# Optimization experiments

Hardware: AMD Instinct MI355X
Metric: run time of the kernel (lower is better)

Reference implementation:

```python
import jax, jax.numpy as jnp
import numpy as np

FEAT = 128 * 4 * 4   # 2048, from input_size=(64,128,4,4)
NCLS = 20            # hard-coded n_classes
S = 0.31             # threshold margin from forward()


def setup_inputs() -> dict:
    key = jax.random.key(0)
    kx, ke, kc, kf = jax.random.split(key, 4)
    x = jax.random.normal(kx, (16384, 128, 4, 4), dtype=jnp.float32)
    # encoder stub: linear 2048 -> 2048
    W_enc = jax.random.normal(ke, (FEAT, FEAT), dtype=jnp.float32) * 0.02
    b_enc = jnp.zeros((FEAT,), dtype=jnp.float32)
    # classifier: linear 2048 -> 20
    W_cls = jax.random.normal(kc, (FEAT, NCLS), dtype=jnp.float32) * 0.02
    b_cls = jnp.zeros((NCLS,), dtype=jnp.float32)
    # flow classification head: linear 2048 -> 20 (produces flow_logits)
    W_fl = jax.random.normal(kf, (FEAT, NCLS), dtype=jnp.float32) * 0.02
    b_fl = jnp.zeros((NCLS,), dtype=jnp.float32)
    return {"x": x, "W_enc": W_enc, "b_enc": b_enc,
            "W_cls": W_cls, "b_cls": b_cls, "W_fl": W_fl, "b_fl": b_fl}


def reference(x, W_enc, b_enc, W_cls, b_cls, W_fl, b_fl):
    B = x.shape[0]
    h = x.reshape(B, -1) @ W_enc + b_enc                    # encoder -> [B, 2048]
    cls_preds = jax.nn.softmax(h @ W_cls + b_cls, axis=1)   # [B, 20]
    flow_logits = h @ W_fl + b_fl                           # flow classify head, [B, 20]
    # taus = softmax(flow_logits).min(1); per-row confidence threshold
    tau = jnp.min(jax.nn.softmax(flow_logits, axis=1), axis=1)  # [B]
    predicted = jnp.max(cls_preds, axis=1)                      # [B]
    # original loop: if predicted < tau + s -> zero the row (vectorized here)
    keep = predicted >= tau + S
    return jnp.where(keep[:, None], cls_preds, jnp.zeros((), cls_preds.dtype))
```

## Files before the change

### kernel.cpp

```cpp
#include <hip/hip_runtime.h>
#include <math.h>


typedef float v2f __attribute__((ext_vector_type(2)));
typedef float v4f __attribute__((ext_vector_type(4)));

#define KD    2048
#define NCLS  20
#define NC2   40
#define SMARG 0.31f

#define WEFF_OFF 0
#define BIAS_OFF 81920

#define CHUNK   128
#define XS_STR  132
#define XS_BUF  (64 * XS_STR)
#define HACC_STR 44
#define HACC_WS  (64 * HACC_STR)
#define SMEM_FLOATS 22528

static __device__ __forceinline__ v2f fma2(v2f a, v2f b, v2f c) {
#if __has_builtin(__builtin_elementwise_fma)
    return __builtin_elementwise_fma(a, b, c);
#else
    v2f r; r[0] = fmaf(a[0], b[0], c[0]); r[1] = fmaf(a[1], b[1], c[1]); return r;
#endif
}

__global__ __launch_bounds__(256)
void k0_prep(const float* __restrict__ Wc, const float* __restrict__ bc,
             const float* __restrict__ Wf, const float* __restrict__ bf,
             const float* __restrict__ be, float* __restrict__ ws)
{
    const int b = blockIdx.x;
    const int t = threadIdx.x;
    if (b < 80) {
        v4f z = {0.f, 0.f, 0.f, 0.f};
        *(v4f*)&ws[WEFF_OFF + 4 * (b * 256 + t)] = z;
    } else {
        const int col = b - 80;
        const float* Wp = (col < NCLS) ? Wc : Wf;
        const int cc = (col < NCLS) ? col : col - NCLS;
        float p = 0.f;
        for (int n = t; n < KD; n += 256)
            p = fmaf(be[n], Wp[n * NCLS + cc], p);
        __shared__ float red[256];
        red[t] = p;
        __syncthreads();
        for (int s = 128; s > 0; s >>= 1) {
            if (t < s) red[t] += red[t + s];
            __syncthreads();
        }
        if (t == 0)
            ws[BIAS_OFF + col] = red[0] + ((col < NCLS) ? bc[cc] : bf[cc]);
    }
}

template<int NCHUNKS, int BSTR, bool FUSED>
__global__ __launch_bounds__(1024)
void skinny_gemm(const float* __restrict__ A,
                 const float* __restrict__ B0,
                 const float* __restrict__ B1,
                 float* __restrict__ Cacc,
                 const float* __restrict__ bias2,
                 float* __restrict__ outp)
{
    __shared__ __align__(16) float smem[SMEM_FLOATS];
    const int tid  = threadIdx.x;
    const int lane = tid & 63;
    const int wu   = __builtin_amdgcn_readfirstlane(tid >> 6);
    const int cgu  = wu & 1;
    const int ksu  = wu >> 1;

    int m0, kbase;
    if (FUSED) { m0 = blockIdx.x * 64;        kbase = 0; }
    else       { m0 = (blockIdx.x >> 3) * 64; kbase = (blockIdx.x & 7) * (NCHUNKS * CHUNK); }

    const int lrow = tid >> 4;
    const int lkq  = tid & 15;
    const float* aptr  = A + (size_t)(m0 + lrow) * KD + kbase + 4 * lkq;
    const float* bbase = (cgu ? B1 : B0) + (size_t)(kbase + ksu * (CHUNK / 8)) * BSTR;

    v2f acc[10];
    #pragma unroll
    for (int j = 0; j < 10; ++j) acc[j] = (v2f){0.f, 0.f};

    {
        v4f v0 = *(const v4f*)(aptr);
        v4f v1 = *(const v4f*)(aptr + 64);
        float* xb = smem + lrow * XS_STR;
        *(v4f*)(xb + 4 * lkq)      = v0;
        *(v4f*)(xb + 64 + 4 * lkq) = v1;
    }
    __syncthreads();

    for (int c = 0; c < NCHUNKS; ++c) {
        const int buf = c & 1;
        v4f p0, p1;
        if (c + 1 < NCHUNKS) {
            p0 = *(const v4f*)(aptr + (c + 1) * CHUNK);
            p1 = *(const v4f*)(aptr + (c + 1) * CHUNK + 64);
        }

        const float* xs   = smem + buf * XS_BUF + lane * XS_STR + ksu * (CHUNK / 8);
        const float* brow = bbase + (size_t)c * (CHUNK * BSTR);
        #pragma unroll 2
        for (int q = 0; q < 4; ++q) {
            v4f xv = *(const v4f*)(xs + 4 * q);
            #pragma unroll
            for (int i = 0; i < 4; ++i) {
                v2f xx = { xv[i], xv[i] };
                const float* br = brow + (4 * q + i) * BSTR;
                #pragma unroll
                for (int j = 0; j < 10; ++j)
                    acc[j] = fma2(xx, *(const v2f*)(br + 2 * j), acc[j]);
            }
        }

        if (c + 1 < NCHUNKS) {
            float* xb = smem + (buf ^ 1) * XS_BUF + lrow * XS_STR;
            *(v4f*)(xb + 4 * lkq)      = p0;
            *(v4f*)(xb + 64 + 4 * lkq) = p1;
        }
        __syncthreads();
    }

    float* H = smem;
    {
        float* Hw = H + ksu * HACC_WS + lane * HACC_STR + 20 * cgu;
        #pragma unroll
        for (int j = 0; j < 10; ++j)
            *(v2f*)(Hw + 2 * j) = acc[j];
    }
    __syncthreads();

    if (FUSED) {
        if (tid < 64) {
            v4f l4[10];
            #pragma unroll
            for (int j = 0; j < 10; ++j) {
                v4f s = *(const v4f*)(H + tid * HACC_STR + 4 * j);
                #pragma unroll
                for (int ks = 1; ks < 8; ++ks)
                    s += *(const v4f*)(H + ks * HACC_WS + tid * HACC_STR + 4 * j);
                l4[j] = s + *(const v4f*)(bias2 + 4 * j);
            }
            float mC = l4[0][0];
            #pragma unroll
            for (int j = 0; j < 5; ++j) {
                #pragma unroll
                for (int i = 0; i < 4; ++i) mC = fmaxf(mC, l4[j][i]);
            }
            float e[20];
            float sC = 0.f;
            #pragma unroll
            for (int j = 0; j < 5; ++j) {
                #pragma unroll
                for (int i = 0; i < 4; ++i) {
                    float ev = expf(l4[j][i] - mC);
                    e[4 * j + i] = ev;
                    sC += ev;
                }
            }
            float mF = l4[5][0], mnF = l4[5][0];
            #pragma unroll
            for (int j = 5; j < 10; ++j) {
                #pragma unroll
                for (int i = 0; i < 4; ++i) {
                    float vv = l4[j][i];
                    mF = fmaxf(mF, vv);
                    mnF = fminf(mnF, vv);
                }
            }
            float sF = 0.f;
            #pragma unroll
            for (int j = 5; j < 10; ++j) {
                #pragma unroll
                for (int i = 0; i < 4; ++i) sF += expf(l4[j][i] - mF);
            }
            float pred  = 1.f / sC;
            float tau   = expf(mnF - mF) / sF;
            float scale = (pred >= tau + SMARG) ? pred : 0.f;
            float* op = outp + (size_t)(m0 + tid) * NCLS;
            #pragma unroll
            for (int j = 0; j < 5; ++j) {
                v4f o;
                #pragma unroll
                for (int i = 0; i < 4; ++i) o[i] = e[4 * j + i] * scale;
                *(v4f*)(op + 4 * j) = o;
            }
        }
    } else {
        for (int idx = tid; idx < 64 * NC2; idx += 1024) {
            int row = idx / NC2, cc = idx % NC2;
            float s = 0.f;
            #pragma unroll
            for (int ks = 0; ks < 8; ++ks)
                s += H[ks * HACC_WS + row * HACC_STR + cc];
            atomicAdd(Cacc + (size_t)(m0 + row) * NC2 + cc, s);
        }
    }
}

extern "C" void kernel_launch(void* const* d_in, const int* in_sizes, int n_in,
                              void* d_out, int out_size, void* d_ws, size_t ws_size,
                              hipStream_t stream) {
    const float* X  = (const float*)d_in[0];
    const float* We = (const float*)d_in[1];
    const float* be = (const float*)d_in[2];
    const float* Wc = (const float*)d_in[3];
    const float* bc = (const float*)d_in[4];
    const float* Wf = (const float*)d_in[5];
    const float* bf = (const float*)d_in[6];
    float* out = (float*)d_out;
    float* ws  = (float*)d_ws;
    (void)in_sizes; (void)n_in; (void)out_size; (void)ws_size;

    k0_prep<<<dim3(120), dim3(256), 0, stream>>>(Wc, bc, Wf, bf, be, ws);
    skinny_gemm<2, 20, false><<<dim3(256), dim3(1024), 0, stream>>>(
        We, Wc, Wf, ws + WEFF_OFF, nullptr, nullptr);
    skinny_gemm<16, 40, true><<<dim3(256), dim3(1024), 0, stream>>>(
        X, ws + WEFF_OFF, ws + WEFF_OFF + 20, nullptr, ws + BIAS_OFF, out);
}
```

Measured before the change: 277.3 us.

## Restructure skinny GEMM to stage weight panels in LDS and stream activations from registers

Replaces the old kernel, which staged X tiles in shared memory and read the 40-column weights from global memory, with a panel scheme. Each 512-k slice of the fused weight is transposed into LDS, and each wave keeps four rows of X in registers and reads them straight from global memory with prefetch. Partial sums across lanes are combined by a butterfly shuffle reduction instead of an 8-way shared-memory sum. Blocks now cover 32 rows (512 blocks for the main GEMM), which raises parallelism but adds register pressure from 80 accumulators per thread and more LDS reloads.

Result: slower. 672.5 us (+142.5%).

```diff
diff --git a/kernel.cpp b/kernel.cpp
--- a/kernel.cpp
+++ b/kernel.cpp
@@ -13,12 +13,9 @@
 #define WEFF_OFF 0
 #define BIAS_OFF 81920
 
-#define CHUNK   128
-#define XS_STR  132
-#define XS_BUF  (64 * XS_STR)
-#define HACC_STR 44
-#define HACC_WS  (64 * HACC_STR)
-#define SMEM_FLOATS 22528
+#define PROW  1028
+#define PANEL_FLOATS (20 * PROW)
+#define HROW  164
 
 static __device__ __forceinline__ v2f fma2(v2f a, v2f b, v2f c) {
 #if __has_builtin(__builtin_elementwise_fma)
@@ -57,128 +54,158 @@
     }
 }
 
-template<int NCHUNKS, int BSTR, bool FUSED>
+template<int NSUP, bool FUSED>
 __global__ __launch_bounds__(1024)
-void skinny_gemm(const float* __restrict__ A,
-                 const float* __restrict__ B0,
-                 const float* __restrict__ B1,
-                 float* __restrict__ Cacc,
-                 const float* __restrict__ bias2,
-                 float* __restrict__ outp)
+void panel_gemm(const float* __restrict__ A,
+                const float* __restrict__ B0,
+                const float* __restrict__ B1,
+                float* __restrict__ Cacc,
+                const float* __restrict__ bias2,
+                float* __restrict__ outp)
 {
-    __shared__ __align__(16) float smem[SMEM_FLOATS];
+    __shared__ __align__(16) float smem[PANEL_FLOATS];
     const int tid  = threadIdx.x;
     const int lane = tid & 63;
-    const int wu   = __builtin_amdgcn_readfirstlane(tid >> 6);
-    const int cgu  = wu & 1;
-    const int ksu  = wu >> 1;
+    const int w    = tid >> 6;
+    const int cg   = w & 1;
+    const int rg   = w >> 1;
 
     int m0, kbase;
-    if (FUSED) { m0 = blockIdx.x * 64;        kbase = 0; }
-    else       { m0 = (blockIdx.x >> 3) * 64; kbase = (blockIdx.x & 7) * (NCHUNKS * CHUNK); }
-
-    const int lrow = tid >> 4;
-    const int lkq  = tid & 15;
-    const float* aptr  = A + (size_t)(m0 + lrow) * KD + kbase + 4 * lkq;
-    const float* bbase = (cgu ? B1 : B0) + (size_t)(kbase + ksu * (CHUNK / 8)) * BSTR;
-
-    v2f acc[10];
+    if (FUSED) { m0 = blockIdx.x * 32;              kbase = 0; }
+    else       { m0 = (int)(blockIdx.x >> 2) * 32;  kbase = (int)(blockIdx.x & 3) * 512; }
+
+    const float* Arow = A + (size_t)(m0 + rg * 4) * KD + kbase + 2 * lane;
+
+    v2f acc2[4][10];
     #pragma unroll
-    for (int j = 0; j < 10; ++j) acc[j] = (v2f){0.f, 0.f};
-
+    for (int r = 0; r < 4; ++r)
+        #pragma unroll
+        for (int j = 0; j < 10; ++j) acc2[r][j] = (v2f){0.f, 0.f};
+
+    v2f xv[4], xn[4] = {};
+    #pragma unroll
+    for (int r = 0; r < 4; ++r) xv[r] = *(const v2f*)(Arow + r * KD);
+
+    const int NSTEPS = NSUP * 4;
+    for (int sup = 0; sup < NSUP; ++sup) {
+        if (sup) __syncthreads();
+        {
+            const int kb = kbase + sup * 512;
+            v2f sv[10];
+            #pragma unroll
+            for (int it = 0; it < 10; ++it) {
+                const int pi = tid + it * 1024;
+                const int k = pi / 20, cj = pi % 20;
+                const float* src;
+                if (FUSED) {
+                    src = B0 + (size_t)(kb + k) * 40 + 2 * cj;
+                } else {
+                    src = (cj < 10) ? (B0 + (size_t)(kb + k) * 20 + 2 * cj)
+                                    : (B1 + (size_t)(kb + k) * 20 + 2 * (cj - 10));
+                }
+                sv[it] = *(const v2f*)src;
+            }
+            #pragma unroll
+            for (int it = 0; it < 10; ++it) {
+                const int pi = tid + it * 1024;
+                const int k = pi / 20, cj = pi % 20;
+                *(v2f*)(smem + cj * PROW + 2 * k) = sv[it];
+            }
+        }
+        __syncthreads();
+        #pragma unroll
+        for (int st = 0; st < 4; ++st) {
+            const int step = sup * 4 + st;
+            if (step + 1 < NSTEPS) {
+                #pragma unroll
+                for (int r = 0; r < 4; ++r)
+                    xn[r] = *(const v2f*)(Arow + r * KD + (step + 1) * 128);
+            }
+            const float* pb = smem + cg * (10 * PROW) + st * 256 + 4 * lane;
+            #pragma unroll
+            for (int j2 = 0; j2 < 10; ++j2) {
+                v4f bv  = *(const v4f*)(pb + j2 * PROW);
+                v2f blo = {bv[0], bv[1]}, bhi = {bv[2], bv[3]};
+                #pragma unroll
+                for (int r = 0; r < 4; ++r) {
+                    v2f x0 = {xv[r][0], xv[r][0]};
+                    v2f x1 = {xv[r][1], xv[r][1]};
+                    acc2[r][j2] = fma2(x1, bhi, fma2(x0, blo, acc2[r][j2]));
+                }
+            }
+            #pragma unroll
+            for (int r = 0; r < 4; ++r) xv[r] = xn[r];
+        }
+    }
+
+    __syncthreads();
+    float* v = (float*)acc2;
     {
-        v4f v0 = *(const v4f*)(aptr);
-        v4f v1 = *(const v4f*)(aptr + 64);
-        float* xb = smem + lrow * XS_STR;
-        *(v4f*)(xb + 4 * lkq)      = v0;
-        *(v4f*)(xb + 64 + 4 * lkq) = v1;
+        const bool u1 = lane & 1;
+        #pragma unroll
+        for (int i = 0; i < 40; ++i) {
+            float snd = u1 ? v[i] : v[i + 40];
+            float rcv = __shfl_xor(snd, 1, 64);
+            v[i] = (u1 ? v[i + 40] : v[i]) + rcv;
+        }
+        const bool u2 = lane & 2;
+        #pragma unroll
+        for (int i = 0; i < 20; ++i) {
+            float snd = u2 ? v[i] : v[i + 20];
+            float rcv = __shfl_xor(snd, 2, 64);
+            v[i] = (u2 ? v[i + 20] : v[i]) + rcv;
+        }
+        const bool u4 = lane & 4;
+        #pragma unroll
+        for (int i = 0; i < 10; ++i) {
+            float snd = u4 ? v[i] : v[i + 10];
+            float rcv = __shfl_xor(snd, 4, 64);
+            v[i] = (u4 ? v[i + 10] : v[i]) + rcv;
+        }
+        const bool u8 = lane & 8;
+        #pragma unroll
+        for (int i = 0; i < 5; ++i) {
+            float snd = u8 ? v[i] : v[i + 5];
+            float rcv = __shfl_xor(snd, 8, 64);
+            v[i] = (u8 ? v[i + 5] : v[i]) + rcv;
+        }
+    }
+    {
+        const int g   = lane >> 4;
+        const int r   = 2 * (lane & 1) + ((lane >> 1) & 1);
+        const int cl0 = 10 * ((lane >> 2) & 1) + 5 * ((lane >> 3) & 1);
+        #pragma unroll
+        for (int i = 0; i < 5; ++i)
+            smem[(rg * 4 + r) * HROW + (cg * 20 + cl0 + i) * 4 + g] = v[i];
     }
     __syncthreads();
 
-    for (int c = 0; c < NCHUNKS; ++c) {
-        const int buf = c & 1;
-        v4f p0, p1;
-        if (c + 1 < NCHUNKS) {
-            p0 = *(const v4f*)(aptr + (c + 1) * CHUNK);
-            p1 = *(const v4f*)(aptr + (c + 1) * CHUNK + 64);
-        }
-
-        const float* xs   = smem + buf * XS_BUF + lane * XS_STR + ksu * (CHUNK / 8);
-        const float* brow = bbase + (size_t)c * (CHUNK * BSTR);
-        #pragma unroll 2
-        for (int q = 0; q < 4; ++q) {
-            v4f xv = *(const v4f*)(xs + 4 * q);
-            #pragma unroll
-            for (int i = 0; i < 4; ++i) {
-                v2f xx = { xv[i], xv[i] };
-                const float* br = brow + (4 * q + i) * BSTR;
-                #pragma unroll
-                for (int j = 0; j < 10; ++j)
-                    acc[j] = fma2(xx, *(const v2f*)(br + 2 * j), acc[j]);
-            }
-        }
-
-        if (c + 1 < NCHUNKS) {
-            float* xb = smem + (buf ^ 1) * XS_BUF + lrow * XS_STR;
-            *(v4f*)(xb + 4 * lkq)      = p0;
-            *(v4f*)(xb + 64 + 4 * lkq) = p1;
-        }
-        __syncthreads();
-    }
-
-    float* H = smem;
-    {
-        float* Hw = H + ksu * HACC_WS + lane * HACC_STR + 20 * cgu;
-        #pragma unroll
-        for (int j = 0; j < 10; ++j)
-            *(v2f*)(Hw + 2 * j) = acc[j];
-    }
-    __syncthreads();
-
-    if (FUSED) {
-        if (tid < 64) {
-            v4f l4[10];
-            #pragma unroll
-            for (int j = 0; j < 10; ++j) {
-                v4f s = *(const v4f*)(H + tid * HACC_STR + 4 * j);
-                #pragma unroll
-                for (int ks = 1; ks < 8; ++ks)
-                    s += *(const v4f*)(H + ks * HACC_WS + tid * HACC_STR + 4 * j);
-                l4[j] = s + *(const v4f*)(bias2 + 4 * j);
-            }
-            float mC = l4[0][0];
-            #pragma unroll
-            for (int j = 0; j < 5; ++j) {
-                #pragma unroll
-                for (int i = 0; i < 4; ++i) mC = fmaxf(mC, l4[j][i]);
-            }
+    if (tid < 32) {
+        float l[40];
+        #pragma unroll
+        for (int c = 0; c < 40; ++c) {
+            v4f q = *(const v4f*)(smem + tid * HROW + c * 4);
+            l[c] = (q[0] + q[1]) + (q[2] + q[3]);
+        }
+        if (FUSED) {
+            #pragma unroll
+            for (int c = 0; c < 40; ++c) l[c] += bias2[c];
+            float mC = l[0];
+            #pragma unroll
+            for (int c = 1; c < 20; ++c) mC = fmaxf(mC, l[c]);
             float e[20];
             float sC = 0.f;
             #pragma unroll
-            for (int j = 0; j < 5; ++j) {
-                #pragma unroll
-                for (int i = 0; i < 4; ++i) {
-                    float ev = expf(l4[j][i] - mC);
-                    e[4 * j + i] = ev;
-                    sC += ev;
-                }
-            }
-            float mF = l4[5][0], mnF = l4[5][0];
-            #pragma unroll
-            for (int j = 5; j < 10; ++j) {
-                #pragma unroll
-                for (int i = 0; i < 4; ++i) {
-                    float vv = l4[j][i];
-                    mF = fmaxf(mF, vv);
-                    mnF = fminf(mnF, vv);
-                }
+            for (int c = 0; c < 20; ++c) { e[c] = expf(l[c] - mC); sC += e[c]; }
+            float mF = l[20], mnF = l[20];
+            #pragma unroll
+            for (int c = 21; c < 40; ++c) {
+                mF = fmaxf(mF, l[c]);
+                mnF = fminf(mnF, l[c]);
             }
             float sF = 0.f;
             #pragma unroll
-            for (int j = 5; j < 10; ++j) {
-                #pragma unroll
-                for (int i = 0; i < 4; ++i) sF += expf(l4[j][i] - mF);
-            }
+            for (int c = 20; c < 40; ++c) sF += expf(l[c] - mF);
             float pred  = 1.f / sC;
             float tau   = expf(mnF - mF) / sF;
             float scale = (pred >= tau + SMARG) ? pred : 0.f;
@@ -190,15 +217,10 @@
                 for (int i = 0; i < 4; ++i) o[i] = e[4 * j + i] * scale;
                 *(v4f*)(op + 4 * j) = o;
             }
-        }
-    } else {
-        for (int idx = tid; idx < 64 * NC2; idx += 1024) {
-            int row = idx / NC2, cc = idx % NC2;
-            float s = 0.f;
-            #pragma unroll
-            for (int ks = 0; ks < 8; ++ks)
-                s += H[ks * HACC_WS + row * HACC_STR + cc];
-            atomicAdd(Cacc + (size_t)(m0 + row) * NC2 + cc, s);
+        } else {
+            #pragma unroll
+            for (int c = 0; c < 40; ++c)
+                atomicAdd(Cacc + (size_t)(m0 + tid) * 40 + c, l[c]);
         }
     }
 }
@@ -218,8 +240,8 @@
     (void)in_sizes; (void)n_in; (void)out_size; (void)ws_size;
 
     k0_prep<<<dim3(120), dim3(256), 0, stream>>>(Wc, bc, Wf, bf, be, ws);
-    skinny_gemm<2, 20, false><<<dim3(256), dim3(1024), 0, stream>>>(
+    panel_gemm<1, false><<<dim3(256), dim3(1024), 0, stream>>>(
         We, Wc, Wf, ws + WEFF_OFF, nullptr, nullptr);
-    skinny_gemm<16, 40, true><<<dim3(256), dim3(1024), 0, stream>>>(
-        X, ws + WEFF_OFF, ws + WEFF_OFF + 20, nullptr, ws + BIAS_OFF, out);
-}
+    panel_gemm<4, true><<<dim3(512), dim3(1024), 0, stream>>>(
+        X, ws + WEFF_OFF, nullptr, nullptr, ws + BIAS_OFF, out);
+}
```
